# Performance work log

Measured on AMD Instinct MI355X. Metric: run time of the kernel, lower is better.

Reference implementation:

```python
import jax, jax.numpy as jnp
import numpy as np

VOXEL_SIZE = 96
SHARPNESS = 100.0
EPS = 1e-8


def _grid_coords(V):
    # matches torch: x fastest, normalized by (V-1); shape [V*V, 2] as (x, y)
    y, x = jnp.meshgrid(jnp.arange(V, dtype=jnp.float32), jnp.arange(V, dtype=jnp.float32), indexing='ij')
    return jnp.stack([x.ravel(), y.ravel()], axis=1) / float(V - 1)


def setup_inputs() -> dict:
    key = jax.random.key(0)
    k1, k2, k3 = jax.random.split(key, 3)
    B, N, P = 4, 32, 32
    polygons = jax.random.uniform(k1, (B, N, P, 2), dtype=jnp.float32)
    attributes = jax.random.uniform(k2, (B, 8), dtype=jnp.float32)
    validity_scores = jax.random.uniform(k3, (B, N), dtype=jnp.float32)
    return {"polygons": polygons, "attributes": attributes, "validity_scores": validity_scores}


def _polygon_masks(polygons, coords):
    # polygons: [B,N,P,2], coords: [M,2] -> soft occupancy masks [B,N,M]
    v0 = polygons                              # [B,N,P,2]
    v1 = jnp.roll(polygons, -1, axis=2)        # next vertex (closed loop)
    e = v1 - v0                                # edges [B,N,P,2]
    pts = coords[None, None, None]             # [1,1,1,M,2]
    v = pts - v0[:, :, :, None, :]             # [B,N,P,M,2]
    e_sq = (e * e).sum(-1) + EPS               # [B,N,P]
    t = (v * e[:, :, :, None, :]).sum(-1) / e_sq[..., None]   # [B,N,P,M]
    t = jnp.clip(t, 0.0, 1.0)
    proj = v0[:, :, :, None, :] + t[..., None] * e[:, :, :, None, :]
    diff = pts - proj
    dists = jnp.sqrt((diff * diff).sum(-1))    # [B,N,P,M]
    min_dist = dists.min(axis=2)               # [B,N,M] min over edges
    # ray-casting point-in-polygon (horizontal ray toward +x)
    x_pts = coords[:, 0]                        # [M]
    y_pts = coords[:, 1]
    x0, y0 = v0[..., 0:1], v0[..., 1:2]        # [B,N,P,1]
    x1, y1 = v1[..., 0:1], v1[..., 1:2]
    y_crosses = ((y0 <= y_pts) & (y1 > y_pts)) | ((y1 <= y_pts) & (y0 > y_pts))
    inter_x = x0 + (x1 - x0) * ((y_pts - y0) / (y1 - y0 + EPS))
    crossings = (inter_x > x_pts) & y_crosses  # [B,N,P,M]
    inside = (crossings.sum(axis=2) % 2) == 1  # [B,N,M]
    sdf = jnp.where(inside, -min_dist, min_dist)
    return jax.nn.sigmoid(-sdf * SHARPNESS)    # [B,N,M]


def reference(polygons, attributes, validity_scores):
    B = polygons.shape[0]
    V = VOXEL_SIZE
    coords = _grid_coords(V)                                   # [V*V, 2]
    masks = _polygon_masks(polygons, coords)                   # [B,N,M]
    valid = validity_scores >= 0.5                             # [B,N]
    combined = jnp.max(jnp.where(valid[:, :, None], masks, 0.0), axis=1)  # [B,M]
    combined = combined.reshape(B, V, V)                       # [B,H,W]
    # height extrusion: int(round(clamp(attr,0,1)*D)), clamped to [1,D]; non-differentiable
    norm_h = jnp.clip(attributes[:, 0], 0.0, 1.0)
    hv = jnp.clip(jnp.round(norm_h * V), 1.0, float(V))        # [B]
    hv = jax.lax.stop_gradient(hv)
    depth_mask = (jnp.arange(V, dtype=jnp.float32)[None, :] < hv[:, None]).astype(combined.dtype)  # [B,D]
    voxels = combined[:, None, :, :] * depth_mask[:, :, None, None]  # [B,D,H,W]
    return voxels
```

## Files before the change

### kernel.cpp

```cpp
#include <hip/hip_runtime.h>

#define V 96
#define VV (V * V)
#define B_ 4
#define N_ 32
#define P_ 32
#define BLOCKS_PER_BN (VV / 256)

__global__ __launch_bounds__(256) void mask_kernel(
    const float* __restrict__ poly,
    const float* __restrict__ validity,
    float* __restrict__ combined)
{
    const int bn  = blockIdx.x / BLOCKS_PER_BN;
    const int pix = (blockIdx.x % BLOCKS_PER_BN) * 256 + threadIdx.x;

    if (validity[bn] < 0.5f) return;

    __shared__ float sx0[P_], sy0[P_], sex[P_], sey[P_], srq[P_], sry[P_];
    if (threadIdx.x < P_) {
        const int p  = threadIdx.x;
        const int pn = (p + 1) & (P_ - 1);
        const float* base = poly + (size_t)bn * (P_ * 2);
        float x0 = base[p * 2],  y0 = base[p * 2 + 1];
        float x1 = base[pn * 2], y1 = base[pn * 2 + 1];
        float ex = x1 - x0, ey = y1 - y0;
        sx0[p] = x0; sy0[p] = y0; sex[p] = ex; sey[p] = ey;
        srq[p] = __builtin_amdgcn_rcpf(ex * ex + ey * ey + 1e-8f);
        sry[p] = __builtin_amdgcn_rcpf(ey + 1e-8f);
    }
    __syncthreads();

    const int py_i = pix / V, px_i = pix - py_i * V;
    const float px = (float)px_i / 95.0f;
    const float py = (float)py_i / 95.0f;

    float mind2 = 1e30f;
    int   par   = 0;

    #pragma unroll
    for (int p = 0; p < P_; ++p) {
        const int pn = (p + 1) & (P_ - 1);
        float x0 = sx0[p], y0 = sy0[p];
        float y1 = sy0[pn];
        float ex = sex[p], ey = sey[p];

        float vx = px - x0, vy = py - y0;
        float t  = (vx * ex + vy * ey) * srq[p];
        t = fminf(fmaxf(t, 0.0f), 1.0f);
        float dx = vx - t * ex, dy = vy - t * ey;
        float d2 = dx * dx + dy * dy;
        mind2 = fminf(mind2, d2);

        bool c0 = (y0 <= py);
        bool c1 = (y1 <= py);
        float inter_x = x0 + ex * ((py - y0) * sry[p]);
        par ^= (int)((c0 != c1) & (inter_x > px));
    }

    float mind = sqrtf(mind2);
    float sdf  = par ? -mind : mind;
    float m = 1.0f / (1.0f + __expf(sdf * 100.0f));

    if (m >= 1e-5f) {
        const int b = bn >> 5;
        atomicMax((unsigned int*)(combined + (size_t)b * VV + pix),
                  __float_as_uint(m));
    }
}

__global__ __launch_bounds__(256) void expand_kernel(
    const float* __restrict__ combined,
    const float* __restrict__ attr,
    float4* __restrict__ out)
{
    const int gid = blockIdx.x * 256 + threadIdx.x;
    const int row = gid / (V / 4);
    const int x4  = gid - row * (V / 4);
    const int y   = row % V;
    const int t_  = row / V;
    const int d   = t_ % V;
    const int b   = t_ / V;

    float a  = attr[b * 8];
    float nh = fminf(fmaxf(a, 0.0f), 1.0f);
    float hv = fminf(fmaxf(rintf(nh * (float)V), 1.0f), (float)V);
    float keep = ((float)d < hv) ? 1.0f : 0.0f;

    float4 c = ((const float4*)combined)[(size_t)b * (VV / 4) + y * (V / 4) + x4];
    out[gid] = make_float4(c.x * keep, c.y * keep, c.z * keep, c.w * keep);
}

extern "C" void kernel_launch(void* const* d_in, const int* in_sizes, int n_in,
                              void* d_out, int out_size, void* d_ws, size_t ws_size,
                              hipStream_t stream) {
    const float* polygons = (const float*)d_in[0];
    const float* attrs    = (const float*)d_in[1];
    const float* validity = (const float*)d_in[2];
    float* out = (float*)d_out;
    float* combined = (float*)d_ws;

    hipMemsetAsync(combined, 0, (size_t)B_ * VV * sizeof(float), stream);

    mask_kernel<<<B_ * N_ * BLOCKS_PER_BN, 256, 0, stream>>>(polygons, validity, combined);
    expand_kernel<<<(B_ * V * V * (V / 4)) / 256, 256, 0, stream>>>(combined, attrs, (float4*)out);
}
```

Measured before the change: 72.96 us.

## Group polygons per block, drop atomics and memset, reduce partial maxima in expand

Each mask block now handles 8 polygons of one batch and keeps a running max in registers. It writes one partial plane per group instead of doing atomicMax into a zeroed buffer, which removes the memset launch and the atomic traffic. The expand kernel reads four partial planes and takes their max before writing the extruded volume. Each expand thread now does four reads instead of one. Mask blocks also drop from 4608 to 576, so there is less parallelism, and invalid polygons are skipped inside the loop instead of by an early exit.

Measured after the change: 80.41 us. 10.2% more time.

```diff
diff --git a/kernel.cpp b/kernel.cpp
--- a/kernel.cpp
+++ b/kernel.cpp
@@ -5,29 +5,32 @@
 #define B_ 4
 #define N_ 32
 #define P_ 32
-#define BLOCKS_PER_BN (VV / 256)
+#define G_ 4
+#define NPG (N_ / G_)
+#define TILES (VV / 256)
 
 __global__ __launch_bounds__(256) void mask_kernel(
     const float* __restrict__ poly,
     const float* __restrict__ validity,
-    float* __restrict__ combined)
+    float* __restrict__ combined4)
 {
-    const int bn  = blockIdx.x / BLOCKS_PER_BN;
-    const int pix = (blockIdx.x % BLOCKS_PER_BN) * 256 + threadIdx.x;
+    const int bg  = blockIdx.x / TILES;
+    const int pix = (blockIdx.x % TILES) * 256 + threadIdx.x;
+    const int b   = bg >> 2;
+    const int g   = bg & (G_ - 1);
 
-    if (validity[bn] < 0.5f) return;
-
-    __shared__ float sx0[P_], sy0[P_], sex[P_], sey[P_], srq[P_], sry[P_];
-    if (threadIdx.x < P_) {
-        const int p  = threadIdx.x;
-        const int pn = (p + 1) & (P_ - 1);
-        const float* base = poly + (size_t)bn * (P_ * 2);
+    __shared__ float sx0[NPG][P_], sy0[NPG][P_], sex[NPG][P_], sey[NPG][P_],
+                     srq[NPG][P_], sry[NPG][P_];
+    {
+        const int t  = threadIdx.x;
+        const int nl = t >> 5, p = t & 31, pn = (p + 1) & 31;
+        const float* base = poly + (size_t)(b * N_ + g * NPG + nl) * (P_ * 2);
         float x0 = base[p * 2],  y0 = base[p * 2 + 1];
         float x1 = base[pn * 2], y1 = base[pn * 2 + 1];
         float ex = x1 - x0, ey = y1 - y0;
-        sx0[p] = x0; sy0[p] = y0; sex[p] = ex; sey[p] = ey;
-        srq[p] = __builtin_amdgcn_rcpf(ex * ex + ey * ey + 1e-8f);
-        sry[p] = __builtin_amdgcn_rcpf(ey + 1e-8f);
+        sx0[nl][p] = x0; sy0[nl][p] = y0; sex[nl][p] = ex; sey[nl][p] = ey;
+        srq[nl][p] = __builtin_amdgcn_rcpf(ex * ex + ey * ey + 1e-8f);
+        sry[nl][p] = __builtin_amdgcn_rcpf(ey + 1e-8f);
     }
     __syncthreads();
 
@@ -35,42 +38,41 @@
     const float px = (float)px_i / 95.0f;
     const float py = (float)py_i / 95.0f;
 
-    float mind2 = 1e30f;
-    int   par   = 0;
+    float best = 0.0f;
+    for (int nl = 0; nl < NPG; ++nl) {
+        if (validity[b * N_ + g * NPG + nl] < 0.5f) continue;
 
-    #pragma unroll
-    for (int p = 0; p < P_; ++p) {
-        const int pn = (p + 1) & (P_ - 1);
-        float x0 = sx0[p], y0 = sy0[p];
-        float y1 = sy0[pn];
-        float ex = sex[p], ey = sey[p];
+        float mind2 = 1e30f;
+        int   par   = 0;
+        #pragma unroll
+        for (int p = 0; p < P_; ++p) {
+            const int pn = (p + 1) & (P_ - 1);
+            float x0 = sx0[nl][p], y0 = sy0[nl][p];
+            float y1 = sy0[nl][pn];
+            float ex = sex[nl][p], ey = sey[nl][p];
 
-        float vx = px - x0, vy = py - y0;
-        float t  = (vx * ex + vy * ey) * srq[p];
-        t = fminf(fmaxf(t, 0.0f), 1.0f);
-        float dx = vx - t * ex, dy = vy - t * ey;
-        float d2 = dx * dx + dy * dy;
-        mind2 = fminf(mind2, d2);
+            float vx = px - x0, vy = py - y0;
+            float t  = (vx * ex + vy * ey) * srq[nl][p];
+            t = fminf(fmaxf(t, 0.0f), 1.0f);
+            float dx = vx - t * ex, dy = vy - t * ey;
+            float d2 = dx * dx + dy * dy;
+            mind2 = fminf(mind2, d2);
 
-        bool c0 = (y0 <= py);
-        bool c1 = (y1 <= py);
-        float inter_x = x0 + ex * ((py - y0) * sry[p]);
-        par ^= (int)((c0 != c1) & (inter_x > px));
+            bool c0 = (y0 <= py);
+            bool c1 = (y1 <= py);
+            float inter_x = x0 + ex * (vy * sry[nl][p]);
+            par ^= (int)((c0 != c1) & (inter_x > px));
+        }
+        float mind = sqrtf(mind2);
+        float sdf  = par ? -mind : mind;
+        float m = __builtin_amdgcn_rcpf(1.0f + __expf(sdf * 100.0f));
+        best = fmaxf(best, m);
     }
-
-    float mind = sqrtf(mind2);
-    float sdf  = par ? -mind : mind;
-    float m = 1.0f / (1.0f + __expf(sdf * 100.0f));
-
-    if (m >= 1e-5f) {
-        const int b = bn >> 5;
-        atomicMax((unsigned int*)(combined + (size_t)b * VV + pix),
-                  __float_as_uint(m));
-    }
+    combined4[(size_t)bg * VV + pix] = best;
 }
 
 __global__ __launch_bounds__(256) void expand_kernel(
-    const float* __restrict__ combined,
+    const float* __restrict__ combined4,
     const float* __restrict__ attr,
     float4* __restrict__ out)
 {
@@ -87,8 +89,18 @@
     float hv = fminf(fmaxf(rintf(nh * (float)V), 1.0f), (float)V);
     float keep = ((float)d < hv) ? 1.0f : 0.0f;
 
-    float4 c = ((const float4*)combined)[(size_t)b * (VV / 4) + y * (V / 4) + x4];
-    out[gid] = make_float4(c.x * keep, c.y * keep, c.z * keep, c.w * keep);
+    const float4* c4 = (const float4*)combined4;
+    const int pixoff = y * (V / 4) + x4;
+    float4 c0 = c4[(size_t)(b * G_ + 0) * (VV / 4) + pixoff];
+    float4 c1 = c4[(size_t)(b * G_ + 1) * (VV / 4) + pixoff];
+    float4 c2 = c4[(size_t)(b * G_ + 2) * (VV / 4) + pixoff];
+    float4 c3 = c4[(size_t)(b * G_ + 3) * (VV / 4) + pixoff];
+    float4 r;
+    r.x = fmaxf(fmaxf(c0.x, c1.x), fmaxf(c2.x, c3.x)) * keep;
+    r.y = fmaxf(fmaxf(c0.y, c1.y), fmaxf(c2.y, c3.y)) * keep;
+    r.z = fmaxf(fmaxf(c0.z, c1.z), fmaxf(c2.z, c3.z)) * keep;
+    r.w = fmaxf(fmaxf(c0.w, c1.w), fmaxf(c2.w, c3.w)) * keep;
+    out[gid] = r;
 }
 
 extern "C" void kernel_launch(void* const* d_in, const int* in_sizes, int n_in,
@@ -97,11 +109,9 @@
     const float* polygons = (const float*)d_in[0];
     const float* attrs    = (const float*)d_in[1];
     const float* validity = (const float*)d_in[2];
-    float* out = (float*)d_out;
-    float* combined = (float*)d_ws;
+    float* out       = (float*)d_out;
+    float* combined4 = (float*)d_ws;
 
-    hipMemsetAsync(combined, 0, (size_t)B_ * VV * sizeof(float), stream);
-
-    mask_kernel<<<B_ * N_ * BLOCKS_PER_BN, 256, 0, stream>>>(polygons, validity, combined);
-    expand_kernel<<<(B_ * V * V * (V / 4)) / 256, 256, 0, stream>>>(combined, attrs, (float4*)out);
+    mask_kernel<<<B_ * G_ * TILES, 256, 0, stream>>>(polygons, validity, combined4);
+    expand_kernel<<<(B_ * V * V * (V / 4)) / 256, 256, 0, stream>>>(combined4, attrs, (float4*)out);
 }
```

## Replace atomicMax accumulation with per-polygon partial masks reduced in expand kernel

Applied to the files above, without the earlier changes.

The mask kernel now writes each polygon's soft mask to a per-(batch,polygon) workspace slice instead of doing atomicMax into a shared combined buffer, which also removes the memset launch. The expand kernel reduces the max over valid polygons for one row into shared memory and then writes a quarter of the depth slices for that row. This trades atomic contention and one launch for extra workspace traffic (B*N*VV floats written and re-read, each row read four times). Small arithmetic tweaks swap the division for rcp and reuse vy.

After: 78.02 us. +6.9%, slower.

```diff
diff --git a/kernel.cpp b/kernel.cpp
--- a/kernel.cpp
+++ b/kernel.cpp
@@ -5,15 +5,15 @@
 #define B_ 4
 #define N_ 32
 #define P_ 32
-#define BLOCKS_PER_BN (VV / 256)
+#define TILES (VV / 256)
 
 __global__ __launch_bounds__(256) void mask_kernel(
     const float* __restrict__ poly,
     const float* __restrict__ validity,
-    float* __restrict__ combined)
+    float* __restrict__ partial)
 {
-    const int bn  = blockIdx.x / BLOCKS_PER_BN;
-    const int pix = (blockIdx.x % BLOCKS_PER_BN) * 256 + threadIdx.x;
+    const int bn  = blockIdx.x / TILES;
+    const int pix = (blockIdx.x % TILES) * 256 + threadIdx.x;
 
     if (validity[bn] < 0.5f) return;
 
@@ -37,7 +37,6 @@
 
     float mind2 = 1e30f;
     int   par   = 0;
-
     #pragma unroll
     for (int p = 0; p < P_; ++p) {
         const int pn = (p + 1) & (P_ - 1);
@@ -54,41 +53,60 @@
 
         bool c0 = (y0 <= py);
         bool c1 = (y1 <= py);
-        float inter_x = x0 + ex * ((py - y0) * sry[p]);
+        float inter_x = x0 + ex * (vy * sry[p]);
         par ^= (int)((c0 != c1) & (inter_x > px));
     }
-
     float mind = sqrtf(mind2);
     float sdf  = par ? -mind : mind;
-    float m = 1.0f / (1.0f + __expf(sdf * 100.0f));
+    float m = __builtin_amdgcn_rcpf(1.0f + __expf(sdf * 100.0f));
 
-    if (m >= 1e-5f) {
-        const int b = bn >> 5;
-        atomicMax((unsigned int*)(combined + (size_t)b * VV + pix),
-                  __float_as_uint(m));
-    }
+    partial[(size_t)bn * VV + pix] = m;
 }
 
-__global__ __launch_bounds__(256) void expand_kernel(
-    const float* __restrict__ combined,
+__global__ __launch_bounds__(192) void expand_kernel(
+    const float* __restrict__ partial,
+    const float* __restrict__ validity,
     const float* __restrict__ attr,
     float4* __restrict__ out)
 {
-    const int gid = blockIdx.x * 256 + threadIdx.x;
-    const int row = gid / (V / 4);
-    const int x4  = gid - row * (V / 4);
-    const int y   = row % V;
-    const int t_  = row / V;
-    const int d   = t_ % V;
-    const int b   = t_ / V;
+    const int bid = blockIdx.x;
+    const int b   = bid / (V * 4);
+    const int rem = bid - b * (V * 4);
+    const int y   = rem >> 2;
+    const int q   = rem & 3;
+    const int t   = threadIdx.x;
+
+    __shared__ float red[V];
+
+    if (t < V) {
+        const int x = t;
+        float m = 0.0f;
+        #pragma unroll
+        for (int n = 0; n < N_; ++n) {
+            if (validity[b * N_ + n] >= 0.5f) {
+                m = fmaxf(m, partial[(size_t)(b * N_ + n) * VV + y * V + x]);
+            }
+        }
+        red[x] = m;
+    }
+    __syncthreads();
 
     float a  = attr[b * 8];
     float nh = fminf(fmaxf(a, 0.0f), 1.0f);
     float hv = fminf(fmaxf(rintf(nh * (float)V), 1.0f), (float)V);
-    float keep = ((float)d < hv) ? 1.0f : 0.0f;
 
-    float4 c = ((const float4*)combined)[(size_t)b * (VV / 4) + y * (V / 4) + x4];
-    out[gid] = make_float4(c.x * keep, c.y * keep, c.z * keep, c.w * keep);
+    const float4* red4 = (const float4*)red;
+    #pragma unroll
+    for (int it = 0; it < 3; ++it) {
+        const int idx = it * 192 + t;
+        const int dl  = idx / 24;
+        const int x4  = idx - dl * 24;
+        const int d   = q * 24 + dl;
+        const float keep = ((float)d < hv) ? 1.0f : 0.0f;
+        float4 c = red4[x4];
+        out[((size_t)(b * V + d) * V + y) * (V / 4) + x4] =
+            make_float4(c.x * keep, c.y * keep, c.z * keep, c.w * keep);
+    }
 }
 
 extern "C" void kernel_launch(void* const* d_in, const int* in_sizes, int n_in,
@@ -97,11 +115,9 @@
     const float* polygons = (const float*)d_in[0];
     const float* attrs    = (const float*)d_in[1];
     const float* validity = (const float*)d_in[2];
-    float* out = (float*)d_out;
-    float* combined = (float*)d_ws;
+    float* out     = (float*)d_out;
+    float* partial = (float*)d_ws;
 
-    hipMemsetAsync(combined, 0, (size_t)B_ * VV * sizeof(float), stream);
-
-    mask_kernel<<<B_ * N_ * BLOCKS_PER_BN, 256, 0, stream>>>(polygons, validity, combined);
-    expand_kernel<<<(B_ * V * V * (V / 4)) / 256, 256, 0, stream>>>(combined, attrs, (float4*)out);
+    mask_kernel<<<B_ * N_ * TILES, 256, 0, stream>>>(polygons, validity, partial);
+    expand_kernel<<<B_ * V * 4, 192, 0, stream>>>(partial, validity, attrs, (float4*)out);
 }
```
